# Performance work log

Hardware: AMD Instinct MI355X
Metric: run time of the kernel (lower is better)

Reference implementation:

```python
import jax, jax.numpy as jnp
import numpy as np

THETA = 10.0  # gaussian sharpness from __init__


def _bilinear_align_corners(x, out_h, out_w):
    # torch F.interpolate(mode='bilinear', align_corners=True)
    n, c, H, W = x.shape
    ys = jnp.arange(out_h, dtype=x.dtype) * ((H - 1) / (out_h - 1))
    xs = jnp.arange(out_w, dtype=x.dtype) * ((W - 1) / (out_w - 1))
    y0 = jnp.floor(ys).astype(jnp.int32)
    y1 = jnp.minimum(y0 + 1, H - 1)
    wy = ys - y0.astype(x.dtype)
    x0 = jnp.floor(xs).astype(jnp.int32)
    x1 = jnp.minimum(x0 + 1, W - 1)
    wx = xs - x0.astype(x.dtype)
    top = x[:, :, y0, :]
    bot = x[:, :, y1, :]
    xh = top * (1 - wy)[None, None, :, None] + bot * wy[None, None, :, None]
    left = xh[:, :, :, x0]
    right = xh[:, :, :, x1]
    return left * (1 - wx)[None, None, None, :] + right * wx[None, None, None, :]


def _unfold3x3(x):
    # torch F.unfold(kernel_size=3, padding=1, stride=1).view(n, c, 9, h, w)
    # zero padding; kernel positions in row-major order
    n, c, h, w = x.shape
    p = jnp.pad(x, ((0, 0), (0, 0), (1, 1), (1, 1)))
    patches = [p[:, :, di:di + h, dj:dj + w] for di in range(3) for dj in range(3)]
    return jnp.stack(patches, axis=2)  # [n, c, 9, h, w]


def reference(mask, edge):
    n, c, h, w = mask.shape
    e = _bilinear_align_corners(edge, h, w)          # [n, 1, h, w]
    le = e[:, :, None] - _unfold3x3(e)               # [n, 1, 9, h, w]
    wgt = jax.nn.softmax(-THETA * le * le, axis=2)   # gaussian similarity softmax over 3x3 nbhd
    m = _unfold3x3(mask) * wgt                       # [n, c, 9, h, w]
    return m.sum(axis=2)                             # [n, c, h, w]


def setup_inputs() -> dict:
    key = jax.random.key(0)
    k1, k2 = jax.random.split(key)
    mask = jax.random.normal(k1, (8, 64, 128, 128), dtype=jnp.float32)
    edge = jax.random.normal(k2, (8, 1, 64, 64), dtype=jnp.float32)
    return {"mask": mask, "edge": edge}
```

## Files before the change

kernel.cpp:

```cpp
#include <hip/hip_runtime.h>


#define THETA 10.0f

constexpr int NB = 8;
constexpr int C  = 64;
constexpr int H  = 128, W = 128;
constexpr int EH = 64,  EW = 64;

constexpr int ROWS = 8;
constexpr int CG   = 8;

__global__ __launch_bounds__(256) void geg_kernel(
    const float* __restrict__ mask,
    const float* __restrict__ edge,
    float* __restrict__ out)
{
    __shared__ float e_s[ROWS + 2][W + 4];

    const int t     = threadIdx.x;
    const int cg    = blockIdx.x;
    const int ytile = blockIdx.y;
    const int n     = blockIdx.z;
    const int y0    = ytile * ROWS;

    const int lane = t & 31;
    const int x4   = lane * 4;
    const int r    = t >> 5;
    const int gy   = y0 + r;

    int rowoff[3];
    rowoff[0] = max(gy - 1, 0) * W + x4;
    rowoff[1] = gy * W + x4;
    rowoff[2] = min(gy + 1, H - 1) * W + x4;

    const int c0 = cg * CG;
    const float* mptr = mask + (size_t)(n * C + c0) * (H * W);

    float4 buf[2][3];
    #pragma unroll
    for (int i = 0; i < 3; ++i) {
        buf[0][i] = *(const float4*)(mptr + rowoff[i]);
        buf[1][i] = *(const float4*)(mptr + H * W + rowoff[i]);
    }

    const float* eg = edge + n * (EH * EW);
    const float s = 63.0f / 127.0f;
    for (int idx = t; idx < (ROWS + 2) * (W + 2); idx += 256) {
        int rr = idx / (W + 2);
        int cc = idx - rr * (W + 2);
        int egy = y0 - 1 + rr;
        int egx = cc - 1;
        float v = 0.0f;
        if (egy >= 0 && egy < H && egx >= 0 && egx < W) {
            float ys = egy * s;
            float xs = egx * s;
            float yf = floorf(ys), xf = floorf(xs);
            int iy0 = (int)yf, ix0 = (int)xf;
            int iy1 = min(iy0 + 1, EH - 1), ix1 = min(ix0 + 1, EW - 1);
            float wy = ys - yf, wx = xs - xf;
            float tl = eg[iy0 * EW + ix0], tr = eg[iy0 * EW + ix1];
            float bl = eg[iy1 * EW + ix0], br = eg[iy1 * EW + ix1];
            float lv = tl + (bl - tl) * wy;
            float rv = tr + (br - tr) * wy;
            v = lv + (rv - lv) * wx;
        }
        e_s[rr][cc] = v;
    }
    __syncthreads();

    float w[4][9];
    #pragma unroll
    for (int p = 0; p < 4; ++p) {
        const int gx = x4 + p;
        const float c = e_s[r + 1][gx + 1];
        float a[9], sum = 0.0f;
        #pragma unroll
        for (int di = 0; di < 3; ++di) {
            #pragma unroll
            for (int dj = 0; dj < 3; ++dj) {
                float d = c - e_s[r + di][gx + dj];
                float e = __expf(-THETA * d * d);
                a[di * 3 + dj] = e;
                sum += e;
            }
        }
        const float inv = 1.0f / sum;
        #pragma unroll
        for (int di = 0; di < 3; ++di) {
            #pragma unroll
            for (int dj = 0; dj < 3; ++dj) {
                int ny = gy + di - 1, nx = gx + dj - 1;
                bool ok = (ny >= 0) & (ny < H) & (nx >= 0) & (nx < W);
                w[p][di * 3 + dj] = ok ? a[di * 3 + dj] * inv : 0.0f;
            }
        }
    }

    float* optr = out + (size_t)(n * C + c0) * (H * W) + gy * W + x4;

    #pragma unroll
    for (int ci = 0; ci < CG; ++ci) {
        float4 cur[3];
        #pragma unroll
        for (int i = 0; i < 3; ++i) cur[i] = buf[ci & 1][i];

        if (ci + 2 < CG) {
            #pragma unroll
            for (int i = 0; i < 3; ++i)
                buf[ci & 1][i] = *(const float4*)(mptr + (ci + 2) * (H * W) + rowoff[i]);
        }

        float av[4] = {0.f, 0.f, 0.f, 0.f};
        #pragma unroll
        for (int i = 0; i < 3; ++i) {
            float m6[6];
            m6[0] = __shfl_up(cur[i].w, 1, 32);
            m6[1] = cur[i].x; m6[2] = cur[i].y; m6[3] = cur[i].z; m6[4] = cur[i].w;
            m6[5] = __shfl_down(cur[i].x, 1, 32);
            #pragma unroll
            for (int p = 0; p < 4; ++p) {
                av[p] = fmaf(m6[p + 0], w[p][i * 3 + 0],
                        fmaf(m6[p + 1], w[p][i * 3 + 1],
                        fmaf(m6[p + 2], w[p][i * 3 + 2], av[p])));
            }
        }
        *(float4*)(optr + ci * (H * W)) = make_float4(av[0], av[1], av[2], av[3]);
    }
}

extern "C" void kernel_launch(void* const* d_in, const int* in_sizes, int n_in,
                              void* d_out, int out_size, void* d_ws, size_t ws_size,
                              hipStream_t stream) {
    const float* mask = (const float*)d_in[0];
    const float* edge = (const float*)d_in[1];
    float* out = (float*)d_out;

    dim3 grid(C / CG, H / ROWS, NB);
    dim3 block(256);
    geg_kernel<<<grid, block, 0, stream>>>(mask, edge, out);
}
```

Measured before the change: 84.73 us.

## Stage mask halo tiles in shared memory to remove redundant row loads

Mask rows for four channels at a time (tile rows plus a one-row halo) are loaded cooperatively into shared memory, and each thread reads its 3x3 neighbourhood from there. Before, every thread loaded three rows per channel straight from global memory, reading each row about three times. The next four channels are prefetched into registers while the first four are computed. Horizontal neighbours now come from shared memory instead of wavefront shuffles, and a min-blocks-per-SM hint is added to the launch bounds. This costs about 20KB more shared memory and extra block-wide barriers, which may limit occupancy.

```diff
diff --git a/kernel.cpp b/kernel.cpp
--- a/kernel.cpp
+++ b/kernel.cpp
@@ -7,16 +7,18 @@
 constexpr int C  = 64;
 constexpr int H  = 128, W = 128;
 constexpr int EH = 64,  EW = 64;
+constexpr int HW = H * W;
 
 constexpr int ROWS = 8;
 constexpr int CG   = 8;
 
-__global__ __launch_bounds__(256) void geg_kernel(
+__global__ __launch_bounds__(256, 4) void geg_kernel(
     const float* __restrict__ mask,
     const float* __restrict__ edge,
     float* __restrict__ out)
 {
     __shared__ float e_s[ROWS + 2][W + 4];
+    __shared__ float m_s[4][ROWS + 2][W];
 
     const int t     = threadIdx.x;
     const int cg    = blockIdx.x;
@@ -29,19 +31,22 @@
     const int r    = t >> 5;
     const int gy   = y0 + r;
 
-    int rowoff[3];
-    rowoff[0] = max(gy - 1, 0) * W + x4;
-    rowoff[1] = gy * W + x4;
-    rowoff[2] = min(gy + 1, H - 1) * W + x4;
+    const int wid  = t >> 6;
+    const int li   = t & 63;
+    const int srow = li >> 5;
+    const int scol = (li & 31) * 4;
 
     const int c0 = cg * CG;
-    const float* mptr = mask + (size_t)(n * C + c0) * (H * W);
+    const float* mptr = mask + (size_t)(n * C + c0) * HW;
 
-    float4 buf[2][3];
+    float4 st[5];
+    int goff[5];
     #pragma unroll
-    for (int i = 0; i < 3; ++i) {
-        buf[0][i] = *(const float4*)(mptr + rowoff[i]);
-        buf[1][i] = *(const float4*)(mptr + H * W + rowoff[i]);
+    for (int k = 0; k < 5; ++k) {
+        int row10 = 2 * k + srow;
+        int gr = min(max(y0 - 1 + row10, 0), H - 1);
+        goff[k] = gr * W + scol;
+        st[k] = *(const float4*)(mptr + wid * HW + goff[k]);
     }
 
     const float* eg = edge + n * (EH * EW);
@@ -97,35 +102,60 @@
         }
     }
 
-    float* optr = out + (size_t)(n * C + c0) * (H * W) + gy * W + x4;
+    #pragma unroll
+    for (int k = 0; k < 5; ++k)
+        *(float4*)&m_s[wid][2 * k + srow][scol] = st[k];
+    __syncthreads();
 
     #pragma unroll
-    for (int ci = 0; ci < CG; ++ci) {
-        float4 cur[3];
-        #pragma unroll
-        for (int i = 0; i < 3; ++i) cur[i] = buf[ci & 1][i];
+    for (int k = 0; k < 5; ++k)
+        st[k] = *(const float4*)(mptr + (wid + 4) * HW + goff[k]);
 
-        if (ci + 2 < CG) {
-            #pragma unroll
-            for (int i = 0; i < 3; ++i)
-                buf[ci & 1][i] = *(const float4*)(mptr + (ci + 2) * (H * W) + rowoff[i]);
-        }
+    float* optr = out + (size_t)(n * C + c0) * HW + gy * W + x4;
+    const int xm = max(x4 - 1, 0);
+    const int xp = min(x4 + 4, W - 1);
 
+    #pragma unroll
+    for (int ci = 0; ci < 4; ++ci) {
         float av[4] = {0.f, 0.f, 0.f, 0.f};
         #pragma unroll
-        for (int i = 0; i < 3; ++i) {
-            float m6[6];
-            m6[0] = __shfl_up(cur[i].w, 1, 32);
-            m6[1] = cur[i].x; m6[2] = cur[i].y; m6[3] = cur[i].z; m6[4] = cur[i].w;
-            m6[5] = __shfl_down(cur[i].x, 1, 32);
+        for (int di = 0; di < 3; ++di) {
+            const float* mrow = m_s[ci][r + di];
+            const float4 mid = *(const float4*)(mrow + x4);
+            float m6[6] = { mrow[xm], mid.x, mid.y, mid.z, mid.w, mrow[xp] };
             #pragma unroll
             for (int p = 0; p < 4; ++p) {
-                av[p] = fmaf(m6[p + 0], w[p][i * 3 + 0],
-                        fmaf(m6[p + 1], w[p][i * 3 + 1],
-                        fmaf(m6[p + 2], w[p][i * 3 + 2], av[p])));
+                av[p] = fmaf(m6[p + 0], w[p][di * 3 + 0],
+                        fmaf(m6[p + 1], w[p][di * 3 + 1],
+                        fmaf(m6[p + 2], w[p][di * 3 + 2], av[p])));
             }
         }
-        *(float4*)(optr + ci * (H * W)) = make_float4(av[0], av[1], av[2], av[3]);
+        *(float4*)(optr + ci * HW) = make_float4(av[0], av[1], av[2], av[3]);
+    }
+
+    __syncthreads();
+
+    #pragma unroll
+    for (int k = 0; k < 5; ++k)
+        *(float4*)&m_s[wid][2 * k + srow][scol] = st[k];
+    __syncthreads();
+
+    #pragma unroll
+    for (int ci = 0; ci < 4; ++ci) {
+        float av[4] = {0.f, 0.f, 0.f, 0.f};
+        #pragma unroll
+        for (int di = 0; di < 3; ++di) {
+            const float* mrow = m_s[ci][r + di];
+            const float4 mid = *(const float4*)(mrow + x4);
+            float m6[6] = { mrow[xm], mid.x, mid.y, mid.z, mid.w, mrow[xp] };
+            #pragma unroll
+            for (int p = 0; p < 4; ++p) {
+                av[p] = fmaf(m6[p + 0], w[p][di * 3 + 0],
+                        fmaf(m6[p + 1], w[p][di * 3 + 1],
+                        fmaf(m6[p + 2], w[p][di * 3 + 2], av[p])));
+            }
+        }
+        *(float4*)(optr + (ci + 4) * HW) = make_float4(av[0], av[1], av[2], av[3]);
     }
 }
 
```

Result: slower. 101.4 us (+19.7%).
